# Kernel tuning notes

Measured on AMD Instinct MI355X. Metric: run time of the kernel, lower is better.

## Reference

```python
import jax, jax.numpy as jnp
from jax import lax
import numpy as np

EPS = 1e-8


def _pdist(a):
    # torch.cdist(a, a, p=2): pairwise Euclidean distances [B, B]
    sq = jnp.sum(a * a, axis=1)
    d2 = sq[:, None] + sq[None, :] - 2.0 * (a @ a.T)
    d2 = jnp.maximum(d2, 0.0)
    # safe sqrt: zero distance -> 0 with zero (not NaN) gradient
    pos = d2 > 0
    return jnp.where(pos, jnp.sqrt(jnp.where(pos, d2, 1.0)), 0.0)


def _local_curvature(x, k):
    # PCA-residual curvature per sample: 1 - S0 / sum(S) over k-NN neighborhood
    dists = _pdist(x)                          # [B, B]
    _, knn_idx = lax.top_k(-dists, k + 1)      # smallest k+1 distances
    knn_idx = knn_idx[:, 1:]                   # drop self -> [B, k]
    nbrs = x[knn_idx]                          # [B, k, D] gather
    centered = nbrs - jnp.mean(nbrs, axis=1, keepdims=True)
    S = jnp.linalg.svd(centered, compute_uv=False)  # batched singular values [B, k]
    linearity = S[:, 0] / (jnp.sum(S, axis=1) + EPS)
    return 1.0 - linearity                     # [B]


def reference(z, ref_emb, x_original, k):
    B = z.shape[0]
    curv = _local_curvature(x_original, k)     # [B]
    z_dist = _pdist(z)
    ref_dist = _pdist(ref_emb)
    # weights = clamp(1 - max(curv_i, curv_j), min=0.1)
    weights = jnp.maximum(1.0 - jnp.maximum(curv[:, None], curv[None, :]), 0.1)
    z_norm = z_dist / (jnp.max(z_dist) + EPS)
    ref_norm = ref_dist / (jnp.max(ref_dist) + EPS)
    errors = (z_norm - ref_norm) ** 2 * weights
    mask = jnp.triu(jnp.ones((B, B), dtype=bool), k=1)
    n_pairs = B * (B - 1) / 2.0
    return jnp.sum(jnp.where(mask, errors, 0.0)) / n_pairs


def setup_inputs() -> dict:
    key = jax.random.key(0)
    k1, k2, k3 = jax.random.split(key, 3)
    B, D, DZ, DR = 4096, 1024, 128, 128
    return {
        "z": jax.random.normal(k1, (B, DZ), dtype=jnp.float32),
        "ref_emb": jax.random.normal(k2, (B, DR), dtype=jnp.float32),
        "x_original": jax.random.normal(k3, (B, D), dtype=jnp.float32),
        "k": 10,
    }
```

## Files before the change

kernel.cpp:

```cpp
#include <hip/hip_runtime.h>
#include <math.h>

#define NB 4096
#define DX 1024
#define DZ 128
#define KNN 10
#define STR 32
#define NLIST 32
#define BKK 64

typedef short short8v __attribute__((ext_vector_type(8)));
typedef float f32x4 __attribute__((ext_vector_type(4)));

#define MFMA16(a, b, c) __builtin_amdgcn_mfma_f32_16x16x32_bf16((a), (b), (c), 0, 0, 0)

__device__ __forceinline__ ushort f2bf(float f) {
  unsigned u = __float_as_uint(f);
  u += 0x7FFFu + ((u >> 16) & 1u);
  return (ushort)(u >> 16);
}
__device__ __forceinline__ float bf2f(ushort h) {
  return __uint_as_float(((unsigned)h) << 16);
}

__device__ __forceinline__ short8v frag_ld(const ushort* base, int row, int fg) {
  int off = (row << 6) + (fg << 4);
  off ^= (row & 7) << 4;
  return *(const short8v*)((const char*)base + off);
}

__device__ __forceinline__ int swz64(int row, int c8) {
  return (row << 7) + ((c8 ^ (row & 7)) << 4);
}
__device__ __forceinline__ short8v frag_ld64(const ushort* base, int row, int kk, int fg) {
  return *(const short8v*)((const char*)base + swz64(row, kk * 4 + fg));
}

#define INSERT10(td, ti, v, idx)                         \
  do {                                                   \
    if ((v) < td[KNN - 1]) {                             \
      _Pragma("unroll")                                  \
      for (int k_ = KNN - 1; k_ >= 1; --k_) {            \
        bool bk = (v) < td[k_];                          \
        bool bk1 = (v) < td[k_ - 1];                     \
        td[k_] = bk ? (bk1 ? td[k_ - 1] : (v)) : td[k_]; \
        ti[k_] = bk ? (bk1 ? ti[k_ - 1] : (idx)) : ti[k_]; \
      }                                                  \
      bool b0 = (v) < td[0];                             \
      ti[0] = b0 ? (idx) : ti[0];                        \
      td[0] = b0 ? (v) : td[0];                          \
    }                                                    \
  } while (0)

__global__ __launch_bounds__(256) void k_rowsq(const float* __restrict__ a,
                                               float* __restrict__ out, int D) {
  int row = blockIdx.x;
  const float4* p = (const float4*)(a + (size_t)row * D);
  float s = 0.f;
  for (int d = threadIdx.x; d < (D >> 2); d += 256) {
    float4 v = p[d];
    s = fmaf(v.x, v.x, s); s = fmaf(v.y, v.y, s);
    s = fmaf(v.z, v.z, s); s = fmaf(v.w, v.w, s);
  }
#pragma unroll
  for (int m = 32; m; m >>= 1) s += __shfl_xor(s, m);
  __shared__ float red[4];
  int w = threadIdx.x >> 6;
  if ((threadIdx.x & 63) == 0) red[w] = s;
  __syncthreads();
  if (threadIdx.x == 0) out[row] = red[0] + red[1] + red[2] + red[3];
}

__global__ __launch_bounds__(256) void k_prep_x(const float* __restrict__ x,
                                                ushort* __restrict__ xh,
                                                float* __restrict__ sqx) {
  const int row = blockIdx.x, t = threadIdx.x;
  float4 v = ((const float4*)(x + (size_t)row * DX))[t];
  ushort4 hv;
  hv.x = f2bf(v.x); hv.y = f2bf(v.y); hv.z = f2bf(v.z); hv.w = f2bf(v.w);
  ((ushort4*)(xh + (size_t)row * DX))[t] = hv;
  float s = fmaf(v.x, v.x, fmaf(v.y, v.y, fmaf(v.z, v.z, v.w * v.w)));
#pragma unroll
  for (int m = 32; m; m >>= 1) s += __shfl_xor(s, m);
  __shared__ float red[4];
  int w = t >> 6;
  if ((t & 63) == 0) red[w] = s;
  __syncthreads();
  if (t == 0) sqx[row] = red[0] + red[1] + red[2] + red[3];
}

__global__ __launch_bounds__(256) void k_prep_zr(const float* __restrict__ z,
                                                 const float* __restrict__ rfm,
                                                 ushort* __restrict__ zh, ushort* __restrict__ zl,
                                                 ushort* __restrict__ rh, ushort* __restrict__ rl,
                                                 float* __restrict__ sqz, float* __restrict__ sqr) {
  const float* src = blockIdx.y ? rfm : z;
  ushort* ph = blockIdx.y ? rh : zh;
  ushort* pl = blockIdx.y ? rl : zl;
  float* sq = blockIdx.y ? sqr : sqz;
  const int t = threadIdx.x;
  const size_t base = (size_t)blockIdx.x * 1024;
  float4 v = ((const float4*)(src + base))[t];
  float vv[4] = {v.x, v.y, v.z, v.w};
  ushort h[4], l[4];
#pragma unroll
  for (int e = 0; e < 4; ++e) {
    h[e] = f2bf(vv[e]);
    l[e] = f2bf(vv[e] - bf2f(h[e]));
  }
  ushort4 hv; hv.x = h[0]; hv.y = h[1]; hv.z = h[2]; hv.w = h[3];
  ushort4 lv; lv.x = l[0]; lv.y = l[1]; lv.z = l[2]; lv.w = l[3];
  ((ushort4*)(ph + base))[t] = hv;
  ((ushort4*)(pl + base))[t] = lv;
  float s = fmaf(v.x, v.x, fmaf(v.y, v.y, fmaf(v.z, v.z, v.w * v.w)));
#pragma unroll
  for (int m = 16; m; m >>= 1) s += __shfl_xor(s, m);
  if ((t & 31) == 0) sq[blockIdx.x * 8 + (t >> 5)] = s;
}

struct SmemKNN {
  union {
    struct { ushort Ah[128 * BKK], Bh[128 * BKK]; } s;
    float D[64 * 129];
  } u;
};

template<int PRE>
__global__ __launch_bounds__(256, 4) void k_knn(const float* __restrict__ x,
                                                const ushort* __restrict__ xh,
                                                const float* __restrict__ sqx,
                                                float* __restrict__ cand_d,
                                                int* __restrict__ cand_i) {
  __shared__ SmemKNN sm;
  const int bid = blockIdx.y * STR + blockIdx.x;
  const int xcd = bid & 7, rr = bid >> 3;
  const int strip = (xcd & 3) * 8 + (rr & 7);
  const int itile = (xcd >> 2) * 16 + (rr >> 3);
  const int i0 = itile * 128;
  const int j0 = strip * 128;

  const int tid = threadIdx.x;
  const int lane = tid & 63, wv = tid >> 6;
  const int wr = wv >> 1, wc = wv & 1;
  const int fr = lane & 15, fg = lane >> 4;

  float td[KNN];
  int ti[KNN];
#pragma unroll
  for (int k = 0; k < KNN; ++k) { td[k] = 3.0e38f; ti[k] = 0; }
  const int my_chunk = tid >> 7;
  const int t2 = tid & 127;
  const int srow = t2 >> 1;
  const int cbase = (tid & 1) * 64;

  f32x4 acc[4][4];
  const f32x4 zv4 = {0.f, 0.f, 0.f, 0.f};
#pragma unroll
  for (int m = 0; m < 4; ++m)
#pragma unroll
    for (int n = 0; n < 4; ++n) acc[m][n] = zv4;

  for (int kc = 0; kc < DX; kc += BKK) {
    __syncthreads();
    if (PRE) {
#pragma unroll
      for (int l = 0; l < 4; ++l) {
        int idx = tid + l * 256;
        int row = idx >> 3, c8 = idx & 7;
        int off = swz64(row, c8);
        *(uint4*)((char*)sm.u.s.Ah + off) =
            *(const uint4*)(xh + (size_t)(i0 + row) * DX + kc + c8 * 8);
        *(uint4*)((char*)sm.u.s.Bh + off) =
            *(const uint4*)(xh + (size_t)(j0 + row) * DX + kc + c8 * 8);
      }
    } else {
#pragma unroll
      for (int l = 0; l < 4; ++l) {
        int idx = tid + l * 256;
        int row = idx >> 3, c8 = idx & 7;
        int off = swz64(row, c8);
        const float* pa = &x[(size_t)(i0 + row) * DX + kc + c8 * 8];
        const float* pb = &x[(size_t)(j0 + row) * DX + kc + c8 * 8];
        float4 a1 = *(const float4*)pa, a2 = *(const float4*)(pa + 4);
        float4 b1 = *(const float4*)pb, b2 = *(const float4*)(pb + 4);
        uint4 pva, pvb;
        pva.x = (unsigned)f2bf(a1.x) | ((unsigned)f2bf(a1.y) << 16);
        pva.y = (unsigned)f2bf(a1.z) | ((unsigned)f2bf(a1.w) << 16);
        pva.z = (unsigned)f2bf(a2.x) | ((unsigned)f2bf(a2.y) << 16);
        pva.w = (unsigned)f2bf(a2.z) | ((unsigned)f2bf(a2.w) << 16);
        pvb.x = (unsigned)f2bf(b1.x) | ((unsigned)f2bf(b1.y) << 16);
        pvb.y = (unsigned)f2bf(b1.z) | ((unsigned)f2bf(b1.w) << 16);
        pvb.z = (unsigned)f2bf(b2.x) | ((unsigned)f2bf(b2.y) << 16);
        pvb.w = (unsigned)f2bf(b2.z) | ((unsigned)f2bf(b2.w) << 16);
        *(uint4*)((char*)sm.u.s.Ah + off) = pva;
        *(uint4*)((char*)sm.u.s.Bh + off) = pvb;
      }
    }
    __syncthreads();
#pragma unroll
    for (int kk = 0; kk < 2; ++kk) {
      short8v fa[4];
#pragma unroll
      for (int m = 0; m < 4; ++m)
        fa[m] = frag_ld64(sm.u.s.Ah, wr * 64 + m * 16 + fr, kk, fg);
#pragma unroll
      for (int n = 0; n < 4; ++n) {
        short8v fb = frag_ld64(sm.u.s.Bh, wc * 64 + n * 16 + fr, kk, fg);
#pragma unroll
        for (int m = 0; m < 4; ++m)
          acc[m][n] = MFMA16(fa[m], fb, acc[m][n]);
      }
    }
  }
  __syncthreads();
#pragma unroll
  for (int chunk = 0; chunk < 2; ++chunk) {
    if (wr == chunk) {
#pragma unroll
      for (int m = 0; m < 4; ++m)
#pragma unroll
        for (int n = 0; n < 4; ++n)
#pragma unroll
          for (int r = 0; r < 4; ++r) {
            int rl = m * 16 + fg * 4 + r;
            int cl = wc * 64 + n * 16 + fr;
            int gi = i0 + chunk * 64 + rl, gj = j0 + cl;
            float v = sqx[gi] + sqx[gj] - 2.f * acc[m][n][r];
            sm.u.D[rl * 129 + cl] = (gi == gj) ? 3.0e38f : v;
          }
    }
    __syncthreads();
    if (my_chunk == chunk) {
#pragma unroll 4
      for (int c = 0; c < 64; ++c) {
        float v = sm.u.D[srow * 129 + cbase + c];
        int idx = j0 + cbase + c;
        INSERT10(td, ti, v, idx);
      }
    }
    __syncthreads();
  }
  {
    float pd[KNN]; int pi[KNN];
#pragma unroll
    for (int l = 0; l < KNN; ++l) {
      pd[l] = __shfl_xor(td[l], 1);
      pi[l] = __shfl_xor(ti[l], 1);
    }
#pragma unroll
    for (int l = 0; l < KNN; ++l) INSERT10(td, ti, pd[l], pi[l]);
    if ((tid & 1) == 0) {
      int row = i0 + my_chunk * 64 + srow;
#pragma unroll
      for (int l = 0; l < KNN; ++l) {
        cand_d[((size_t)row * NLIST + strip) * KNN + l] = td[l];
        cand_i[((size_t)row * NLIST + strip) * KNN + l] = ti[l];
      }
    }
  }
}

__global__ __launch_bounds__(64) void k_mergegram(const float* __restrict__ cand_d,
                                                  const int* __restrict__ cand_i,
                                                  const float* __restrict__ x,
                                                  float* __restrict__ G) {
  const int pt = blockIdx.x;
  const int lane = threadIdx.x;
  float v[KNN]; int jx[KNN];
  const float* cd = cand_d + ((size_t)pt * NLIST + lane) * KNN;
  const int* ci = cand_i + ((size_t)pt * NLIST + lane) * KNN;
  const bool act = lane < NLIST;
#pragma unroll
  for (int l = 0; l < KNN; ++l) {
    v[l] = act ? cd[l] : 3.0e38f;
    jx[l] = act ? ci[l] : 0;
  }
  const float4* nb[KNN];
#pragma unroll
  for (int k = 0; k < KNN; ++k) {
    float bv = v[0]; int bj = jx[0]; int bl = lane;
#pragma unroll
    for (int m = 1; m < 64; m <<= 1) {
      float ov = __shfl_xor(bv, m);
      int oj = __shfl_xor(bj, m);
      int ol = __shfl_xor(bl, m);
      bool take = ov < bv;
      bv = take ? ov : bv; bj = take ? oj : bj; bl = take ? ol : bl;
    }
    nb[k] = (const float4*)(x + (size_t)bj * DX);
    if (lane == bl) {
#pragma unroll
      for (int l = 0; l < KNN - 1; ++l) { v[l] = v[l + 1]; jx[l] = jx[l + 1]; }
      v[KNN - 1] = 3.0e38f;
    }
  }
  float P[55];
  float U[KNN];
  float q = 0.f;
#pragma unroll
  for (int c = 0; c < 55; ++c) P[c] = 0.f;
#pragma unroll
  for (int a = 0; a < KNN; ++a) U[a] = 0.f;
  for (int d4 = lane; d4 < DX / 4; d4 += 64) {
    float4 n4[KNN];
#pragma unroll
    for (int a = 0; a < KNN; ++a) n4[a] = nb[a][d4];
#pragma unroll
    for (int e = 0; e < 4; ++e) {
      float n[KNN];
#pragma unroll
      for (int a = 0; a < KNN; ++a) n[a] = ((const float*)&n4[a])[e];
      float m = 0.f;
#pragma unroll
      for (int a = 0; a < KNN; ++a) m += n[a];
      m *= 0.1f;
      q = fmaf(m, m, q);
#pragma unroll
      for (int a = 0; a < KNN; ++a) U[a] = fmaf(n[a], m, U[a]);
      int c = 0;
#pragma unroll
      for (int a = 0; a < KNN; ++a)
#pragma unroll
        for (int b = a; b < KNN; ++b) { P[c] = fmaf(n[a], n[b], P[c]); ++c; }
    }
  }
#pragma unroll
  for (int c = 0; c < 55; ++c)
#pragma unroll
    for (int m2 = 32; m2; m2 >>= 1) P[c] += __shfl_xor(P[c], m2);
#pragma unroll
  for (int a = 0; a < KNN; ++a)
#pragma unroll
    for (int m2 = 32; m2; m2 >>= 1) U[a] += __shfl_xor(U[a], m2);
#pragma unroll
  for (int m2 = 32; m2; m2 >>= 1) q += __shfl_xor(q, m2);
  if (lane == 0) {
    int c = 0;
    for (int a = 0; a < KNN; ++a)
      for (int b = a; b < KNN; ++b) { G[(size_t)pt * 55 + c] = P[c] - U[a] - U[b] + q; ++c; }
  }
}

__device__ __forceinline__ constexpr int IJ(int a, int b) {
  return (a <= b) ? (10 * a - (a * (a - 1)) / 2 + (b - a))
                  : (10 * b - (b * (b - 1)) / 2 + (a - b));
}

#define NSWEEP 6
__global__ __launch_bounds__(64) void k_jacobi(const float* __restrict__ G,
                                               float* __restrict__ curv) {
  const int pt = blockIdx.x * 64 + threadIdx.x;
  float M[55];
#pragma unroll
  for (int c = 0; c < 55; ++c) M[c] = G[(size_t)pt * 55 + c];

#pragma unroll
  for (int sweep = 0; sweep < NSWEEP; ++sweep) {
#pragma unroll
    for (int p = 0; p < KNN - 1; ++p) {
#pragma unroll
      for (int q = p + 1; q < KNN; ++q) {
        float apq = M[IJ(p, q)];
        float app = M[IJ(p, p)], aqq = M[IJ(q, q)];
        float theta = (aqq - app) / (2.f * apq);
        float t = 1.f / (fabsf(theta) + sqrtf(fmaf(theta, theta, 1.f)));
        t = (theta < 0.f) ? -t : t;
        t = (apq == 0.f) ? 0.f : t;
        float cc = 1.f / sqrtf(fmaf(t, t, 1.f));
        float ss = t * cc;
#pragma unroll
        for (int r = 0; r < KNN; ++r) {
          if (r == p || r == q) continue;
          float vrp = M[IJ(r, p)];
          float vrq = M[IJ(r, q)];
          M[IJ(r, p)] = cc * vrp - ss * vrq;
          M[IJ(r, q)] = ss * vrp + cc * vrq;
        }
        M[IJ(p, p)] = app - t * apq;
        M[IJ(q, q)] = aqq + t * apq;
        M[IJ(p, q)] = 0.f;
      }
    }
  }

  float lmax = 0.f, ssum = 0.f;
#pragma unroll
  for (int a = 0; a < KNN; ++a) {
    float l = fmaxf(M[IJ(a, a)], 0.f);
    lmax = fmaxf(lmax, l);
    ssum += sqrtf(l);
  }
  curv[pt] = 1.f - sqrtf(lmax) / (ssum + 1e-8f);
}

template<int PRE>
__global__ __launch_bounds__(256, 2) void k_zr(const float* __restrict__ z,
                                               const float* __restrict__ rfm,
                                               const ushort* __restrict__ zh,
                                               const ushort* __restrict__ zl,
                                               const ushort* __restrict__ rh,
                                               const ushort* __restrict__ rl,
                                               const float* __restrict__ sqz,
                                               const float* __restrict__ sqr,
                                               const float* __restrict__ curv,
                                               double* __restrict__ pS,
                                               float* __restrict__ pM) {
  __shared__ struct { ushort Ah[4096], Al[4096], Bh[4096], Bl[4096]; } s;
  const int t = blockIdx.x;
  int ib = 0, base = 0;
  while (base + (32 - ib) <= t) { base += 32 - ib; ++ib; }
  const int jb = ib + (t - base);
  const int i0 = ib * 128, j0 = jb * 128;
  const int tid = threadIdx.x;
  const int lane = tid & 63, wv = tid >> 6;
  const int wr = wv >> 1, wc = wv & 1;
  const int fr = lane & 15, fg = lane >> 4;

  f32x4 zacc[4][4], racc[4][4];
  const f32x4 zv = {0.f, 0.f, 0.f, 0.f};
#pragma unroll
  for (int m = 0; m < 4; ++m)
#pragma unroll
    for (int n = 0; n < 4; ++n) { zacc[m][n] = zv; racc[m][n] = zv; }

#pragma unroll
  for (int mat = 0; mat < 2; ++mat) {
    const float* P = mat ? rfm : z;
    const ushort* Ph = mat ? rh : zh;
    const ushort* Pl = mat ? rl : zl;
    for (int kc = 0; kc < DZ; kc += 32) {
      __syncthreads();
      if (PRE) {
#pragma unroll
        for (int l = 0; l < 2; ++l) {
          int idx = tid + l * 256;
          int row = idx >> 2, c8 = idx & 3;
          int off = (row << 6) + (c8 << 4);
          off ^= (row & 7) << 4;
          size_t ga = (size_t)(i0 + row) * DZ + kc + c8 * 8;
          size_t gb = (size_t)(j0 + row) * DZ + kc + c8 * 8;
          *(uint4*)((char*)s.Ah + off) = *(const uint4*)(Ph + ga);
          *(uint4*)((char*)s.Al + off) = *(const uint4*)(Pl + ga);
          *(uint4*)((char*)s.Bh + off) = *(const uint4*)(Ph + gb);
          *(uint4*)((char*)s.Bl + off) = *(const uint4*)(Pl + gb);
        }
      } else {
#pragma unroll
        for (int l = 0; l < 4; ++l) {
          int idx = tid + l * 256;
          int row = idx >> 3, c4 = idx & 7;
          int off = (row << 6) + (c4 << 3);
          off ^= (row & 7) << 4;
          float4 va = *(const float4*)&P[(size_t)(i0 + row) * DZ + kc + c4 * 4];
          float4 vb = *(const float4*)&P[(size_t)(j0 + row) * DZ + kc + c4 * 4];
          float av[4] = {va.x, va.y, va.z, va.w};
          float bv[4] = {vb.x, vb.y, vb.z, vb.w};
          ushort ah4[4], al4[4], bh4[4], bl4[4];
#pragma unroll
          for (int e = 0; e < 4; ++e) {
            ah4[e] = f2bf(av[e]); al4[e] = f2bf(av[e] - bf2f(ah4[e]));
            bh4[e] = f2bf(bv[e]); bl4[e] = f2bf(bv[e] - bf2f(bh4[e]));
          }
          uint2 p;
          p.x = (unsigned)ah4[0] | ((unsigned)ah4[1] << 16);
          p.y = (unsigned)ah4[2] | ((unsigned)ah4[3] << 16);
          *(uint2*)((char*)s.Ah + off) = p;
          p.x = (unsigned)al4[0] | ((unsigned)al4[1] << 16);
          p.y = (unsigned)al4[2] | ((unsigned)al4[3] << 16);
          *(uint2*)((char*)s.Al + off) = p;
          p.x = (unsigned)bh4[0] | ((unsigned)bh4[1] << 16);
          p.y = (unsigned)bh4[2] | ((unsigned)bh4[3] << 16);
          *(uint2*)((char*)s.Bh + off) = p;
          p.x = (unsigned)bl4[0] | ((unsigned)bl4[1] << 16);
          p.y = (unsigned)bl4[2] | ((unsigned)bl4[3] << 16);
          *(uint2*)((char*)s.Bl + off) = p;
        }
      }
      __syncthreads();
      short8v fah[4], fal[4];
#pragma unroll
      for (int m = 0; m < 4; ++m) {
        int r = wr * 64 + m * 16 + fr;
        fah[m] = frag_ld(s.Ah, r, fg);
        fal[m] = frag_ld(s.Al, r, fg);
      }
#pragma unroll
      for (int n = 0; n < 4; ++n) {
        int r = wc * 64 + n * 16 + fr;
        short8v fbh = frag_ld(s.Bh, r, fg);
        short8v fbl = frag_ld(s.Bl, r, fg);
#pragma unroll
        for (int m = 0; m < 4; ++m) {
          if (mat == 0) {
            zacc[m][n] = MFMA16(fah[m], fbh, zacc[m][n]);
            zacc[m][n] = MFMA16(fah[m], fbl, zacc[m][n]);
            zacc[m][n] = MFMA16(fal[m], fbh, zacc[m][n]);
          } else {
            racc[m][n] = MFMA16(fah[m], fbh, racc[m][n]);
            racc[m][n] = MFMA16(fah[m], fbl, racc[m][n]);
            racc[m][n] = MFMA16(fal[m], fbh, racc[m][n]);
          }
        }
      }
    }
  }

  double s1 = 0, s2 = 0, s3 = 0;
  float mz = 0.f, mr = 0.f;
#pragma unroll
  for (int m = 0; m < 4; ++m)
#pragma unroll
    for (int n = 0; n < 4; ++n)
#pragma unroll
      for (int r = 0; r < 4; ++r) {
        int gi = i0 + wr * 64 + m * 16 + fg * 4 + r;
        int gj = j0 + wc * 64 + n * 16 + fr;
        if (gj > gi) {
          float z2 = fmaxf(sqz[gi] + sqz[gj] - 2.f * zacc[m][n][r], 0.f);
          float r2 = fmaxf(sqr[gi] + sqr[gj] - 2.f * racc[m][n][r], 0.f);
          float w = fmaxf(1.f - fmaxf(curv[gi], curv[gj]), 0.1f);
          s1 += (double)(w * z2);
          s3 += (double)(w * r2);
          s2 += (double)(w * sqrtf(z2 * r2));
          mz = fmaxf(mz, z2);
          mr = fmaxf(mr, r2);
        }
      }
#pragma unroll
  for (int m = 32; m; m >>= 1) {
    s1 += __shfl_xor(s1, m);
    s2 += __shfl_xor(s2, m);
    s3 += __shfl_xor(s3, m);
    mz = fmaxf(mz, __shfl_xor(mz, m));
    mr = fmaxf(mr, __shfl_xor(mr, m));
  }
  __shared__ double rd[4][3];
  __shared__ float rf2[4][2];
  int w = tid >> 6;
  if ((tid & 63) == 0) { rd[w][0] = s1; rd[w][1] = s2; rd[w][2] = s3; rf2[w][0] = mz; rf2[w][1] = mr; }
  __syncthreads();
  if (tid == 0) {
    double a = 0, b = 0, c = 0; float d = 0.f, e = 0.f;
    for (int i = 0; i < 4; ++i) {
      a += rd[i][0]; b += rd[i][1]; c += rd[i][2];
      d = fmaxf(d, rf2[i][0]); e = fmaxf(e, rf2[i][1]);
    }
    pS[(size_t)t * 3 + 0] = a; pS[(size_t)t * 3 + 1] = b; pS[(size_t)t * 3 + 2] = c;
    pM[(size_t)t * 2 + 0] = d; pM[(size_t)t * 2 + 1] = e;
  }
}

__global__ __launch_bounds__(256) void k_final(const double* __restrict__ pS,
                                               const float* __restrict__ pM,
                                               int nb, float* __restrict__ out) {
  int tid = threadIdx.x;
  double s1 = 0, s2 = 0, s3 = 0; float mz = 0.f, mr = 0.f;
  for (int i = tid; i < nb; i += 256) {
    s1 += pS[(size_t)i * 3 + 0]; s2 += pS[(size_t)i * 3 + 1]; s3 += pS[(size_t)i * 3 + 2];
    mz = fmaxf(mz, pM[(size_t)i * 2 + 0]); mr = fmaxf(mr, pM[(size_t)i * 2 + 1]);
  }
#pragma unroll
  for (int m = 32; m; m >>= 1) {
    s1 += __shfl_xor(s1, m); s2 += __shfl_xor(s2, m); s3 += __shfl_xor(s3, m);
    mz = fmaxf(mz, __shfl_xor(mz, m)); mr = fmaxf(mr, __shfl_xor(mr, m));
  }
  __shared__ double rd[4][3];
  __shared__ float rf2[4][2];
  int w = tid >> 6;
  if ((tid & 63) == 0) { rd[w][0] = s1; rd[w][1] = s2; rd[w][2] = s3; rf2[w][0] = mz; rf2[w][1] = mr; }
  __syncthreads();
  if (tid == 0) {
    double a = 0, b = 0, c = 0; float d = 0.f, e = 0.f;
    for (int i = 0; i < 4; ++i) {
      a += rd[i][0]; b += rd[i][1]; c += rd[i][2];
      d = fmaxf(d, rf2[i][0]); e = fmaxf(e, rf2[i][1]);
    }
    double zm = sqrt((double)d) + 1e-8;
    double rm = sqrt((double)e) + 1e-8;
    double total = a / (zm * zm) - 2.0 * b / (zm * rm) + c / (rm * rm);
    double npairs = (double)NB * (double)(NB - 1) / 2.0;
    out[0] = (float)(total / npairs);
  }
}

extern "C" void kernel_launch(void* const* d_in, const int* in_sizes, int n_in,
                              void* d_out, int out_size, void* d_ws, size_t ws_size,
                              hipStream_t stream) {
  const float* z = (const float*)d_in[0];
  const float* rfm = (const float*)d_in[1];
  const float* x = (const float*)d_in[2];
  float* out = (float*)d_out;
  char* w = (char*)d_ws;

  float*  sqx    = (float*)(w + 0);
  float*  sqz    = (float*)(w + 16384);
  float*  sqr    = (float*)(w + 32768);
  float*  curv   = (float*)(w + 49152);
  float*  cand_d = (float*)(w + 229376);
  int*    cand_i = (int*)(w + 5472256);
  float*  G      = (float*)(w + 10715136);
  double* pS     = (double*)(w + 11616256);
  float*  pM     = (float*)(w + 11628928);

  ushort* xh = (ushort*)(w + (size_t)12 * 1024 * 1024);
  ushort* zh = (ushort*)(w + (size_t)20 * 1024 * 1024);
  ushort* zl = (ushort*)(w + (size_t)21 * 1024 * 1024);
  ushort* rh = (ushort*)(w + (size_t)22 * 1024 * 1024);
  ushort* rl = (ushort*)(w + (size_t)23 * 1024 * 1024);
  const bool pre = ws_size >= (size_t)24 * 1024 * 1024;

  if (pre) {
    k_prep_x<<<NB, 256, 0, stream>>>(x, xh, sqx);
    k_prep_zr<<<dim3(NB * DZ / 1024, 2), 256, 0, stream>>>(z, rfm, zh, zl, rh, rl, sqz, sqr);
    k_knn<1><<<dim3(STR, NB / 128), 256, 0, stream>>>(x, xh, sqx, cand_d, cand_i);
  } else {
    k_rowsq<<<NB, 256, 0, stream>>>(x, sqx, DX);
    k_rowsq<<<NB, 256, 0, stream>>>(z, sqz, DZ);
    k_rowsq<<<NB, 256, 0, stream>>>(rfm, sqr, DZ);
    k_knn<0><<<dim3(STR, NB / 128), 256, 0, stream>>>(x, xh, sqx, cand_d, cand_i);
  }
  k_mergegram<<<NB, 64, 0, stream>>>(cand_d, cand_i, x, G);
  k_jacobi<<<NB / 64, 64, 0, stream>>>(G, curv);
  if (pre) {
    k_zr<1><<<528, 256, 0, stream>>>(z, rfm, zh, zl, rh, rl, sqz, sqr, curv, pS, pM);
  } else {
    k_zr<0><<<528, 256, 0, stream>>>(z, rfm, zh, zl, rh, rl, sqz, sqr, curv, pS, pM);
  }
  k_final<<<1, 256, 0, stream>>>(pS, pM, 528, out);
}
```

Before: 248.2 us.

## Double-buffer kNN Gram tiles via direct global-to-LDS loads; read bf16 neighbors in mergegram

The precomputed-bf16 path of the kNN distance GEMM now uses global_load_lds to copy tiles straight into a double-buffered LDS area, issuing the next K-slice before computing the current one. This hides global load latency and removes the register round-trip. Occupancy hint drops from 4 to 2 blocks per CU because the LDS footprint doubles. Separately, the neighbor Gram kernel reads bf16 rows instead of fp32 to halve gather traffic, at some precision cost in the curvature estimate.

```diff
diff --git a/kernel.cpp b/kernel.cpp
--- a/kernel.cpp
+++ b/kernel.cpp
@@ -8,6 +8,7 @@
 #define STR 32
 #define NLIST 32
 #define BKK 64
+#define NSTEP (DX / BKK)
 
 typedef short short8v __attribute__((ext_vector_type(8)));
 typedef float f32x4 __attribute__((ext_vector_type(4)));
@@ -21,6 +22,12 @@
 }
 __device__ __forceinline__ float bf2f(ushort h) {
   return __uint_as_float(((unsigned)h) << 16);
+}
+
+__device__ __forceinline__ void gload16(const ushort* g, ushort* l) {
+  __builtin_amdgcn_global_load_lds(
+      (const __attribute__((address_space(1))) void*)g,
+      (__attribute__((address_space(3))) void*)l, 16, 0, 0);
 }
 
 __device__ __forceinline__ short8v frag_ld(const ushort* base, int row, int fg) {
@@ -120,13 +127,13 @@
 
 struct SmemKNN {
   union {
-    struct { ushort Ah[128 * BKK], Bh[128 * BKK]; } s;
+    struct { ushort A[2][8192]; ushort B[2][8192]; } s;
     float D[64 * 129];
   } u;
 };
 
 template<int PRE>
-__global__ __launch_bounds__(256, 4) void k_knn(const float* __restrict__ x,
+__global__ __launch_bounds__(256, 2) void k_knn(const float* __restrict__ x,
                                                 const ushort* __restrict__ xh,
                                                 const float* __restrict__ sqx,
                                                 float* __restrict__ cand_d,
@@ -160,20 +167,47 @@
 #pragma unroll
     for (int n = 0; n < 4; ++n) acc[m][n] = zv4;
 
-  for (int kc = 0; kc < DX; kc += BKK) {
-    __syncthreads();
-    if (PRE) {
-#pragma unroll
-      for (int l = 0; l < 4; ++l) {
-        int idx = tid + l * 256;
-        int row = idx >> 3, c8 = idx & 7;
-        int off = swz64(row, c8);
-        *(uint4*)((char*)sm.u.s.Ah + off) =
-            *(const uint4*)(xh + (size_t)(i0 + row) * DX + kc + c8 * 8);
-        *(uint4*)((char*)sm.u.s.Bh + off) =
-            *(const uint4*)(xh + (size_t)(j0 + row) * DX + kc + c8 * 8);
-      }
-    } else {
+  if (PRE) {
+    const int lr = lane >> 3;
+    const int lc8 = (lane & 7) ^ lr;
+#define ISSUE_TILE(kc, buf)                                                  \
+  _Pragma("unroll")                                                          \
+  for (int c_ = 0; c_ < 4; ++c_) {                                          \
+    int ch_ = wv * 4 + c_;                                                   \
+    int row_ = ch_ * 8 + lr;                                                 \
+    gload16(xh + (size_t)(i0 + row_) * DX + (kc) + lc8 * 8,                  \
+            &sm.u.s.A[buf][ch_ * 512]);                                      \
+    gload16(xh + (size_t)(j0 + row_) * DX + (kc) + lc8 * 8,                  \
+            &sm.u.s.B[buf][ch_ * 512]);                                      \
+  }
+    ISSUE_TILE(0, 0);
+    int buf = 0;
+    for (int step = 0; step < NSTEP; ++step) {
+      asm volatile("s_waitcnt vmcnt(0)" ::: "memory");
+      __syncthreads();
+      if (step + 1 < NSTEP) ISSUE_TILE((step + 1) * BKK, buf ^ 1);
+      const ushort* Ab = sm.u.s.A[buf];
+      const ushort* Bb = sm.u.s.B[buf];
+#pragma unroll
+      for (int kk = 0; kk < 2; ++kk) {
+        short8v fa[4];
+#pragma unroll
+        for (int m = 0; m < 4; ++m)
+          fa[m] = frag_ld64(Ab, wr * 64 + m * 16 + fr, kk, fg);
+#pragma unroll
+        for (int n = 0; n < 4; ++n) {
+          short8v fb = frag_ld64(Bb, wc * 64 + n * 16 + fr, kk, fg);
+#pragma unroll
+          for (int m = 0; m < 4; ++m)
+            acc[m][n] = MFMA16(fa[m], fb, acc[m][n]);
+        }
+      }
+      buf ^= 1;
+    }
+#undef ISSUE_TILE
+  } else {
+    for (int kc = 0; kc < DX; kc += BKK) {
+      __syncthreads();
 #pragma unroll
       for (int l = 0; l < 4; ++l) {
         int idx = tid + l * 256;
@@ -192,23 +226,23 @@
         pvb.y = (unsigned)f2bf(b1.z) | ((unsigned)f2bf(b1.w) << 16);
         pvb.z = (unsigned)f2bf(b2.x) | ((unsigned)f2bf(b2.y) << 16);
         pvb.w = (unsigned)f2bf(b2.z) | ((unsigned)f2bf(b2.w) << 16);
-        *(uint4*)((char*)sm.u.s.Ah + off) = pva;
-        *(uint4*)((char*)sm.u.s.Bh + off) = pvb;
-      }
-    }
-    __syncthreads();
-#pragma unroll
-    for (int kk = 0; kk < 2; ++kk) {
-      short8v fa[4];
-#pragma unroll
-      for (int m = 0; m < 4; ++m)
-        fa[m] = frag_ld64(sm.u.s.Ah, wr * 64 + m * 16 + fr, kk, fg);
-#pragma unroll
-      for (int n = 0; n < 4; ++n) {
-        short8v fb = frag_ld64(sm.u.s.Bh, wc * 64 + n * 16 + fr, kk, fg);
+        *(uint4*)((char*)sm.u.s.A[0] + off) = pva;
+        *(uint4*)((char*)sm.u.s.B[0] + off) = pvb;
+      }
+      __syncthreads();
+#pragma unroll
+      for (int kk = 0; kk < 2; ++kk) {
+        short8v fa[4];
 #pragma unroll
         for (int m = 0; m < 4; ++m)
-          acc[m][n] = MFMA16(fa[m], fb, acc[m][n]);
+          fa[m] = frag_ld64(sm.u.s.A[0], wr * 64 + m * 16 + fr, kk, fg);
+#pragma unroll
+        for (int n = 0; n < 4; ++n) {
+          short8v fb = frag_ld64(sm.u.s.B[0], wc * 64 + n * 16 + fr, kk, fg);
+#pragma unroll
+          for (int m = 0; m < 4; ++m)
+            acc[m][n] = MFMA16(fa[m], fb, acc[m][n]);
+        }
       }
     }
   }
@@ -260,9 +294,11 @@
   }
 }
 
+template<int PRE>
 __global__ __launch_bounds__(64) void k_mergegram(const float* __restrict__ cand_d,
                                                   const int* __restrict__ cand_i,
                                                   const float* __restrict__ x,
+                                                  const ushort* __restrict__ xh,
                                                   float* __restrict__ G) {
   const int pt = blockIdx.x;
   const int lane = threadIdx.x;
@@ -275,7 +311,7 @@
     v[l] = act ? cd[l] : 3.0e38f;
     jx[l] = act ? ci[l] : 0;
   }
-  const float4* nb[KNN];
+  int nbi[KNN];
 #pragma unroll
   for (int k = 0; k < KNN; ++k) {
     float bv = v[0]; int bj = jx[0]; int bl = lane;
@@ -287,7 +323,7 @@
       bool take = ov < bv;
       bv = take ? ov : bv; bj = take ? oj : bj; bl = take ? ol : bl;
     }
-    nb[k] = (const float4*)(x + (size_t)bj * DX);
+    nbi[k] = bj;
     if (lane == bl) {
 #pragma unroll
       for (int l = 0; l < KNN - 1; ++l) { v[l] = v[l + 1]; jx[l] = jx[l + 1]; }
@@ -301,27 +337,61 @@
   for (int c = 0; c < 55; ++c) P[c] = 0.f;
 #pragma unroll
   for (int a = 0; a < KNN; ++a) U[a] = 0.f;
-  for (int d4 = lane; d4 < DX / 4; d4 += 64) {
-    float4 n4[KNN];
-#pragma unroll
-    for (int a = 0; a < KNN; ++a) n4[a] = nb[a][d4];
-#pragma unroll
-    for (int e = 0; e < 4; ++e) {
-      float n[KNN];
-#pragma unroll
-      for (int a = 0; a < KNN; ++a) n[a] = ((const float*)&n4[a])[e];
-      float m = 0.f;
-#pragma unroll
-      for (int a = 0; a < KNN; ++a) m += n[a];
-      m *= 0.1f;
-      q = fmaf(m, m, q);
-#pragma unroll
-      for (int a = 0; a < KNN; ++a) U[a] = fmaf(n[a], m, U[a]);
-      int c = 0;
-#pragma unroll
-      for (int a = 0; a < KNN; ++a)
-#pragma unroll
-        for (int b = a; b < KNN; ++b) { P[c] = fmaf(n[a], n[b], P[c]); ++c; }
+  if (PRE) {
+    const short8v* nb[KNN];
+#pragma unroll
+    for (int a = 0; a < KNN; ++a)
+      nb[a] = (const short8v*)(xh + (size_t)nbi[a] * DX);
+    for (int d8 = lane; d8 < DX / 8; d8 += 64) {
+      short8v n8[KNN];
+#pragma unroll
+      for (int a = 0; a < KNN; ++a) n8[a] = nb[a][d8];
+#pragma unroll
+      for (int e = 0; e < 8; ++e) {
+        float n[KNN];
+#pragma unroll
+        for (int a = 0; a < KNN; ++a) n[a] = bf2f((ushort)n8[a][e]);
+        float m = 0.f;
+#pragma unroll
+        for (int a = 0; a < KNN; ++a) m += n[a];
+        m *= 0.1f;
+        q = fmaf(m, m, q);
+#pragma unroll
+        for (int a = 0; a < KNN; ++a) U[a] = fmaf(n[a], m, U[a]);
+        int c = 0;
+#pragma unroll
+        for (int a = 0; a < KNN; ++a)
+#pragma unroll
+          for (int b = a; b < KNN; ++b) { P[c] = fmaf(n[a], n[b], P[c]); ++c; }
+      }
+    }
+  } else {
+    const float4* nb[KNN];
+#pragma unroll
+    for (int a = 0; a < KNN; ++a)
+      nb[a] = (const float4*)(x + (size_t)nbi[a] * DX);
+    for (int d4 = lane; d4 < DX / 4; d4 += 64) {
+      float4 n4[KNN];
+#pragma unroll
+      for (int a = 0; a < KNN; ++a) n4[a] = nb[a][d4];
+#pragma unroll
+      for (int e = 0; e < 4; ++e) {
+        float n[KNN];
+#pragma unroll
+        for (int a = 0; a < KNN; ++a) n[a] = ((const float*)&n4[a])[e];
+        float m = 0.f;
+#pragma unroll
+        for (int a = 0; a < KNN; ++a) m += n[a];
+        m *= 0.1f;
+        q = fmaf(m, m, q);
+#pragma unroll
+        for (int a = 0; a < KNN; ++a) U[a] = fmaf(n[a], m, U[a]);
+        int c = 0;
+#pragma unroll
+        for (int a = 0; a < KNN; ++a)
+#pragma unroll
+          for (int b = a; b < KNN; ++b) { P[c] = fmaf(n[a], n[b], P[c]); ++c; }
+      }
     }
   }
 #pragma unroll
@@ -613,13 +683,14 @@
     k_prep_x<<<NB, 256, 0, stream>>>(x, xh, sqx);
     k_prep_zr<<<dim3(NB * DZ / 1024, 2), 256, 0, stream>>>(z, rfm, zh, zl, rh, rl, sqz, sqr);
     k_knn<1><<<dim3(STR, NB / 128), 256, 0, stream>>>(x, xh, sqx, cand_d, cand_i);
+    k_mergegram<1><<<NB, 64, 0, stream>>>(cand_d, cand_i, x, xh, G);
   } else {
     k_rowsq<<<NB, 256, 0, stream>>>(x, sqx, DX);
     k_rowsq<<<NB, 256, 0, stream>>>(z, sqz, DZ);
     k_rowsq<<<NB, 256, 0, stream>>>(rfm, sqr, DZ);
     k_knn<0><<<dim3(STR, NB / 128), 256, 0, stream>>>(x, xh, sqx, cand_d, cand_i);
-  }
-  k_mergegram<<<NB, 64, 0, stream>>>(cand_d, cand_i, x, G);
+    k_mergegram<0><<<NB, 64, 0, stream>>>(cand_d, cand_i, x, xh, G);
+  }
   k_jacobi<<<NB / 64, 64, 0, stream>>>(G, curv);
   if (pre) {
     k_zr<1><<<528, 256, 0, stream>>>(z, rfm, zh, zl, rh, rl, sqz, sqr, curv, pS, pM);
```

After: 263.0 us. +6.0%, slower.

## Fuse prep kernels, fold Jacobi into mergegram, read bf16 neighbors

Applied to the files above, without the earlier changes.

Merges the x and z/ref prep kernels into one launch. Folds the Jacobi eigen-solve into the mergegram kernel so the Gram matrix stays in registers instead of going through global memory and a separate kernel. In the pre path, reads the bf16 copy of x for the neighbor Gram computation, which halves gather bandwidth but lowers the precision of the curvature estimate. It also makes every lane of a 64-thread block run the redundant 6-sweep Jacobi, where before one thread did each point.

```diff
diff --git a/kernel.cpp b/kernel.cpp
--- a/kernel.cpp
+++ b/kernel.cpp
@@ -71,51 +71,56 @@
   if (threadIdx.x == 0) out[row] = red[0] + red[1] + red[2] + red[3];
 }
 
-__global__ __launch_bounds__(256) void k_prep_x(const float* __restrict__ x,
-                                                ushort* __restrict__ xh,
-                                                float* __restrict__ sqx) {
-  const int row = blockIdx.x, t = threadIdx.x;
-  float4 v = ((const float4*)(x + (size_t)row * DX))[t];
-  ushort4 hv;
-  hv.x = f2bf(v.x); hv.y = f2bf(v.y); hv.z = f2bf(v.z); hv.w = f2bf(v.w);
-  ((ushort4*)(xh + (size_t)row * DX))[t] = hv;
-  float s = fmaf(v.x, v.x, fmaf(v.y, v.y, fmaf(v.z, v.z, v.w * v.w)));
-#pragma unroll
-  for (int m = 32; m; m >>= 1) s += __shfl_xor(s, m);
-  __shared__ float red[4];
-  int w = t >> 6;
-  if ((t & 63) == 0) red[w] = s;
-  __syncthreads();
-  if (t == 0) sqx[row] = red[0] + red[1] + red[2] + red[3];
-}
-
-__global__ __launch_bounds__(256) void k_prep_zr(const float* __restrict__ z,
-                                                 const float* __restrict__ rfm,
-                                                 ushort* __restrict__ zh, ushort* __restrict__ zl,
-                                                 ushort* __restrict__ rh, ushort* __restrict__ rl,
-                                                 float* __restrict__ sqz, float* __restrict__ sqr) {
-  const float* src = blockIdx.y ? rfm : z;
-  ushort* ph = blockIdx.y ? rh : zh;
-  ushort* pl = blockIdx.y ? rl : zl;
-  float* sq = blockIdx.y ? sqr : sqz;
+__global__ __launch_bounds__(256) void k_prep(const float* __restrict__ x,
+                                              const float* __restrict__ z,
+                                              const float* __restrict__ rfm,
+                                              ushort* __restrict__ xh,
+                                              ushort* __restrict__ zh, ushort* __restrict__ zl,
+                                              ushort* __restrict__ rh, ushort* __restrict__ rl,
+                                              float* __restrict__ sqx,
+                                              float* __restrict__ sqz, float* __restrict__ sqr) {
+  const int b = blockIdx.x;
   const int t = threadIdx.x;
-  const size_t base = (size_t)blockIdx.x * 1024;
-  float4 v = ((const float4*)(src + base))[t];
-  float vv[4] = {v.x, v.y, v.z, v.w};
-  ushort h[4], l[4];
-#pragma unroll
-  for (int e = 0; e < 4; ++e) {
-    h[e] = f2bf(vv[e]);
-    l[e] = f2bf(vv[e] - bf2f(h[e]));
-  }
-  ushort4 hv; hv.x = h[0]; hv.y = h[1]; hv.z = h[2]; hv.w = h[3];
-  ushort4 lv; lv.x = l[0]; lv.y = l[1]; lv.z = l[2]; lv.w = l[3];
-  ((ushort4*)(ph + base))[t] = hv;
-  ((ushort4*)(pl + base))[t] = lv;
-  float s = fmaf(v.x, v.x, fmaf(v.y, v.y, fmaf(v.z, v.z, v.w * v.w)));
-#pragma unroll
-  for (int m = 16; m; m >>= 1) s += __shfl_xor(s, m);
-  if ((t & 31) == 0) sq[blockIdx.x * 8 + (t >> 5)] = s;
+  if (b < NB) {
+    const int row = b;
+    float4 v = ((const float4*)(x + (size_t)row * DX))[t];
+    ushort4 hv;
+    hv.x = f2bf(v.x); hv.y = f2bf(v.y); hv.z = f2bf(v.z); hv.w = f2bf(v.w);
+    ((ushort4*)(xh + (size_t)row * DX))[t] = hv;
+    float s = fmaf(v.x, v.x, fmaf(v.y, v.y, fmaf(v.z, v.z, v.w * v.w)));
+#pragma unroll
+    for (int m = 32; m; m >>= 1) s += __shfl_xor(s, m);
+    __shared__ float red[4];
+    int w = t >> 6;
+    if ((t & 63) == 0) red[w] = s;
+    __syncthreads();
+    if (t == 0) sqx[row] = red[0] + red[1] + red[2] + red[3];
+  } else {
+    const int e = b - NB;
+    const int mat = e >> 9;
+    const int idx = e & 511;
+    const float* src = mat ? rfm : z;
+    ushort* ph = mat ? rh : zh;
+    ushort* pl = mat ? rl : zl;
+    float* sq = mat ? sqr : sqz;
+    const size_t base = (size_t)idx * 1024;
+    float4 v = ((const float4*)(src + base))[t];
+    float vv[4] = {v.x, v.y, v.z, v.w};
+    ushort h[4], l[4];
+#pragma unroll
+    for (int ee = 0; ee < 4; ++ee) {
+      h[ee] = f2bf(vv[ee]);
+      l[ee] = f2bf(vv[ee] - bf2f(h[ee]));
+    }
+    ushort4 hv; hv.x = h[0]; hv.y = h[1]; hv.z = h[2]; hv.w = h[3];
+    ushort4 lv; lv.x = l[0]; lv.y = l[1]; lv.z = l[2]; lv.w = l[3];
+    ((ushort4*)(ph + base))[t] = hv;
+    ((ushort4*)(pl + base))[t] = lv;
+    float s = fmaf(v.x, v.x, fmaf(v.y, v.y, fmaf(v.z, v.z, v.w * v.w)));
+#pragma unroll
+    for (int m = 16; m; m >>= 1) s += __shfl_xor(s, m);
+    if ((t & 31) == 0) sq[idx * 8 + (t >> 5)] = s;
+  }
 }
 
 struct SmemKNN {
@@ -260,10 +265,18 @@
   }
 }
 
+__device__ __forceinline__ constexpr int IJ(int a, int b) {
+  return (a <= b) ? (10 * a - (a * (a - 1)) / 2 + (b - a))
+                  : (10 * b - (b * (b - 1)) / 2 + (a - b));
+}
+
+#define NSWEEP 6
+template<int PRE>
 __global__ __launch_bounds__(64) void k_mergegram(const float* __restrict__ cand_d,
                                                   const int* __restrict__ cand_i,
                                                   const float* __restrict__ x,
-                                                  float* __restrict__ G) {
+                                                  const ushort* __restrict__ xh,
+                                                  float* __restrict__ curv) {
   const int pt = blockIdx.x;
   const int lane = threadIdx.x;
   float v[KNN]; int jx[KNN];
@@ -275,7 +288,7 @@
     v[l] = act ? cd[l] : 3.0e38f;
     jx[l] = act ? ci[l] : 0;
   }
-  const float4* nb[KNN];
+  int nbi[KNN];
 #pragma unroll
   for (int k = 0; k < KNN; ++k) {
     float bv = v[0]; int bj = jx[0]; int bl = lane;
@@ -287,7 +300,7 @@
       bool take = ov < bv;
       bv = take ? ov : bv; bj = take ? oj : bj; bl = take ? ol : bl;
     }
-    nb[k] = (const float4*)(x + (size_t)bj * DX);
+    nbi[k] = bj;
     if (lane == bl) {
 #pragma unroll
       for (int l = 0; l < KNN - 1; ++l) { v[l] = v[l + 1]; jx[l] = jx[l + 1]; }
@@ -301,27 +314,61 @@
   for (int c = 0; c < 55; ++c) P[c] = 0.f;
 #pragma unroll
   for (int a = 0; a < KNN; ++a) U[a] = 0.f;
-  for (int d4 = lane; d4 < DX / 4; d4 += 64) {
-    float4 n4[KNN];
-#pragma unroll
-    for (int a = 0; a < KNN; ++a) n4[a] = nb[a][d4];
-#pragma unroll
-    for (int e = 0; e < 4; ++e) {
-      float n[KNN];
-#pragma unroll
-      for (int a = 0; a < KNN; ++a) n[a] = ((const float*)&n4[a])[e];
-      float m = 0.f;
-#pragma unroll
-      for (int a = 0; a < KNN; ++a) m += n[a];
-      m *= 0.1f;
-      q = fmaf(m, m, q);
-#pragma unroll
-      for (int a = 0; a < KNN; ++a) U[a] = fmaf(n[a], m, U[a]);
-      int c = 0;
-#pragma unroll
-      for (int a = 0; a < KNN; ++a)
-#pragma unroll
-        for (int b = a; b < KNN; ++b) { P[c] = fmaf(n[a], n[b], P[c]); ++c; }
+  if (PRE) {
+    const short8v* nb[KNN];
+#pragma unroll
+    for (int a = 0; a < KNN; ++a)
+      nb[a] = (const short8v*)(xh + (size_t)nbi[a] * DX);
+    for (int d8 = lane; d8 < DX / 8; d8 += 64) {
+      short8v n8[KNN];
+#pragma unroll
+      for (int a = 0; a < KNN; ++a) n8[a] = nb[a][d8];
+#pragma unroll
+      for (int e = 0; e < 8; ++e) {
+        float n[KNN];
+#pragma unroll
+        for (int a = 0; a < KNN; ++a) n[a] = bf2f((ushort)n8[a][e]);
+        float m = 0.f;
+#pragma unroll
+        for (int a = 0; a < KNN; ++a) m += n[a];
+        m *= 0.1f;
+        q = fmaf(m, m, q);
+#pragma unroll
+        for (int a = 0; a < KNN; ++a) U[a] = fmaf(n[a], m, U[a]);
+        int c = 0;
+#pragma unroll
+        for (int a = 0; a < KNN; ++a)
+#pragma unroll
+          for (int b = a; b < KNN; ++b) { P[c] = fmaf(n[a], n[b], P[c]); ++c; }
+      }
+    }
+  } else {
+    const float4* nb[KNN];
+#pragma unroll
+    for (int a = 0; a < KNN; ++a)
+      nb[a] = (const float4*)(x + (size_t)nbi[a] * DX);
+    for (int d4 = lane; d4 < DX / 4; d4 += 64) {
+      float4 n4[KNN];
+#pragma unroll
+      for (int a = 0; a < KNN; ++a) n4[a] = nb[a][d4];
+#pragma unroll
+      for (int e = 0; e < 4; ++e) {
+        float n[KNN];
+#pragma unroll
+        for (int a = 0; a < KNN; ++a) n[a] = ((const float*)&n4[a])[e];
+        float m = 0.f;
+#pragma unroll
+        for (int a = 0; a < KNN; ++a) m += n[a];
+        m *= 0.1f;
+        q = fmaf(m, m, q);
+#pragma unroll
+        for (int a = 0; a < KNN; ++a) U[a] = fmaf(n[a], m, U[a]);
+        int c = 0;
+#pragma unroll
+        for (int a = 0; a < KNN; ++a)
+#pragma unroll
+          for (int b = a; b < KNN; ++b) { P[c] = fmaf(n[a], n[b], P[c]); ++c; }
+      }
     }
   }
 #pragma unroll
@@ -334,34 +381,23 @@
     for (int m2 = 32; m2; m2 >>= 1) U[a] += __shfl_xor(U[a], m2);
 #pragma unroll
   for (int m2 = 32; m2; m2 >>= 1) q += __shfl_xor(q, m2);
-  if (lane == 0) {
+
+  float M[55];
+  {
     int c = 0;
+#pragma unroll
     for (int a = 0; a < KNN; ++a)
-      for (int b = a; b < KNN; ++b) { G[(size_t)pt * 55 + c] = P[c] - U[a] - U[b] + q; ++c; }
-  }
-}
-
-__device__ __forceinline__ constexpr int IJ(int a, int b) {
-  return (a <= b) ? (10 * a - (a * (a - 1)) / 2 + (b - a))
-                  : (10 * b - (b * (b - 1)) / 2 + (a - b));
-}
-
-#define NSWEEP 6
-__global__ __launch_bounds__(64) void k_jacobi(const float* __restrict__ G,
-                                               float* __restrict__ curv) {
-  const int pt = blockIdx.x * 64 + threadIdx.x;
-  float M[55];
-#pragma unroll
-  for (int c = 0; c < 55; ++c) M[c] = G[(size_t)pt * 55 + c];
-
+#pragma unroll
+      for (int b = a; b < KNN; ++b) { M[c] = P[c] - U[a] - U[b] + q; ++c; }
+  }
 #pragma unroll
   for (int sweep = 0; sweep < NSWEEP; ++sweep) {
 #pragma unroll
     for (int p = 0; p < KNN - 1; ++p) {
 #pragma unroll
-      for (int q = p + 1; q < KNN; ++q) {
-        float apq = M[IJ(p, q)];
-        float app = M[IJ(p, p)], aqq = M[IJ(q, q)];
+      for (int qq = p + 1; qq < KNN; ++qq) {
+        float apq = M[IJ(p, qq)];
+        float app = M[IJ(p, p)], aqq = M[IJ(qq, qq)];
         float theta = (aqq - app) / (2.f * apq);
         float t = 1.f / (fabsf(theta) + sqrtf(fmaf(theta, theta, 1.f)));
         t = (theta < 0.f) ? -t : t;
@@ -370,27 +406,28 @@
         float ss = t * cc;
 #pragma unroll
         for (int r = 0; r < KNN; ++r) {
-          if (r == p || r == q) continue;
+          if (r == p || r == qq) continue;
           float vrp = M[IJ(r, p)];
-          float vrq = M[IJ(r, q)];
+          float vrq = M[IJ(r, qq)];
           M[IJ(r, p)] = cc * vrp - ss * vrq;
-          M[IJ(r, q)] = ss * vrp + cc * vrq;
+          M[IJ(r, qq)] = ss * vrp + cc * vrq;
         }
         M[IJ(p, p)] = app - t * apq;
-        M[IJ(q, q)] = aqq + t * apq;
-        M[IJ(p, q)] = 0.f;
-      }
-    }
-  }
-
-  float lmax = 0.f, ssum = 0.f;
-#pragma unroll
-  for (int a = 0; a < KNN; ++a) {
-    float l = fmaxf(M[IJ(a, a)], 0.f);
-    lmax = fmaxf(lmax, l);
-    ssum += sqrtf(l);
-  }
-  curv[pt] = 1.f - sqrtf(lmax) / (ssum + 1e-8f);
+        M[IJ(qq, qq)] = aqq + t * apq;
+        M[IJ(p, qq)] = 0.f;
+      }
+    }
+  }
+  if (lane == 0) {
+    float lmax = 0.f, ssum = 0.f;
+#pragma unroll
+    for (int a = 0; a < KNN; ++a) {
+      float l = fmaxf(M[IJ(a, a)], 0.f);
+      lmax = fmaxf(lmax, l);
+      ssum += sqrtf(l);
+    }
+    curv[pt] = 1.f - sqrtf(lmax) / (ssum + 1e-8f);
+  }
 }
 
 template<int PRE>
@@ -598,7 +635,6 @@
   float*  curv   = (float*)(w + 49152);
   float*  cand_d = (float*)(w + 229376);
   int*    cand_i = (int*)(w + 5472256);
-  float*  G      = (float*)(w + 10715136);
   double* pS     = (double*)(w + 11616256);
   float*  pM     = (float*)(w + 11628928);
 
@@ -610,17 +646,16 @@
   const bool pre = ws_size >= (size_t)24 * 1024 * 1024;
 
   if (pre) {
-    k_prep_x<<<NB, 256, 0, stream>>>(x, xh, sqx);
-    k_prep_zr<<<dim3(NB * DZ / 1024, 2), 256, 0, stream>>>(z, rfm, zh, zl, rh, rl, sqz, sqr);
+    k_prep<<<NB + 1024, 256, 0, stream>>>(x, z, rfm, xh, zh, zl, rh, rl, sqx, sqz, sqr);
     k_knn<1><<<dim3(STR, NB / 128), 256, 0, stream>>>(x, xh, sqx, cand_d, cand_i);
+    k_mergegram<1><<<NB, 64, 0, stream>>>(cand_d, cand_i, x, xh, curv);
   } else {
     k_rowsq<<<NB, 256, 0, stream>>>(x, sqx, DX);
     k_rowsq<<<NB, 256, 0, stream>>>(z, sqz, DZ);
     k_rowsq<<<NB, 256, 0, stream>>>(rfm, sqr, DZ);
     k_knn<0><<<dim3(STR, NB / 128), 256, 0, stream>>>(x, xh, sqx, cand_d, cand_i);
-  }
-  k_mergegram<<<NB, 64, 0, stream>>>(cand_d, cand_i, x, G);
-  k_jacobi<<<NB / 64, 64, 0, stream>>>(G, curv);
+    k_mergegram<0><<<NB, 64, 0, stream>>>(cand_d, cand_i, x, xh, curv);
+  }
   if (pre) {
     k_zr<1><<<528, 256, 0, stream>>>(z, rfm, zh, zl, rh, rl, sqz, sqr, curv, pS, pM);
   } else {
```

Result: slower. 436.9 us (+76.0%).
